# Kernel optimization log

Hardware: AMD Instinct MI355X
Metric: run time of the kernel (lower is better)

Reference implementation:

```python
import jax, jax.numpy as jnp
import numpy as np

N_HEADS = 2
HEAD_DIM = 32
SCALE = HEAD_DIM ** -0.5


def group_linear(x, w):
    # x: (S, B, din), w: (n_blocks, din_b, dout_b) block-diagonal linear
    S, B, _ = x.shape
    nb, din_b, dout_b = w.shape
    xb = x.reshape(S, B, nb, din_b)
    yb = jnp.einsum('sbnd,nde->sbne', xb, w)
    return yb.reshape(S, B, nb * dout_b)


def setup_inputs() -> dict:
    key = jax.random.key(0)
    ks = jax.random.split(key, 5)
    S, B, dim, nb = 2048, 16, 1024, 8
    block_din = dim // nb          # 128
    emb_b = HEAD_DIM * N_HEADS     # 64 per block
    x = jax.random.normal(ks[0], (S, B, dim), dtype=jnp.float32)
    wq = 0.01 * jax.random.normal(ks[1], (nb, block_din, emb_b), dtype=jnp.float32)
    wk = 0.01 * jax.random.normal(ks[2], (nb, block_din, emb_b), dtype=jnp.float32)
    wv = 0.01 * jax.random.normal(ks[3], (nb, block_din, emb_b), dtype=jnp.float32)
    wf = 0.01 * jax.random.normal(ks[4], (nb, emb_b, block_din), dtype=jnp.float32)
    return {'x': x, 'wq': wq, 'wk': wk, 'wv': wv, 'wf': wf}


def reference(x, wq, wk, wv, wf):
    S, B, dim = x.shape
    nb = wq.shape[0]
    # block-diagonal QKV projections -> (S, B, nb, n_heads, head_dim)
    q = group_linear(x, wq).reshape(S, B, nb, N_HEADS, HEAD_DIM)
    k = group_linear(x, wk).reshape(S, B, nb, N_HEADS, HEAD_DIM)
    v = group_linear(x, wv).reshape(S, B, nb, N_HEADS, HEAD_DIM)
    # attention over the n_blocks axis; heads leading: (S, B, h, nb, hd)
    q = jnp.swapaxes(q, 2, 3) * SCALE
    k = jnp.swapaxes(k, 2, 3)
    v = jnp.swapaxes(v, 2, 3)
    score = jnp.einsum('sbhnd,sbhmd->sbhnm', q, k)  # (S,B,h,nb,nb)
    score = jax.nn.softmax(score, axis=-1)
    out = jnp.einsum('sbhnm,sbhmd->sbhnd', score, v)
    out = jnp.swapaxes(out, 2, 3).reshape(S, B, nb * N_HEADS * HEAD_DIM)
    out = group_linear(out, wf)
    return out.reshape(S, B, dim)
```

## Files before the change

kernel.cpp:

```cpp
#include <hip/hip_runtime.h>
#include <math.h>

using short8  = __attribute__((ext_vector_type(8))) short;
using ushort8 = __attribute__((ext_vector_type(8))) unsigned short;
using f32x4   = __attribute__((ext_vector_type(4))) float;

constexpr int DIM = 1024, NB = 8, NH = 2, HD = 32;
constexpr float SCALE = 0.17677669529663687f;
constexpr int SXW = 1032;
constexpr int SQW = 1544;

__device__ __forceinline__ unsigned short f2bf(float f) {
  unsigned u = __float_as_uint(f);
  u += 0x7fff + ((u >> 16) & 1);
  return (unsigned short)(u >> 16);
}
__device__ __forceinline__ float bf2f(unsigned short h) {
  return __uint_as_float((unsigned)h << 16);
}

__global__ __launch_bounds__(256) void prep_weights(
    const float* __restrict__ wq, const float* __restrict__ wk,
    const float* __restrict__ wv, const float* __restrict__ wf,
    unsigned short* __restrict__ ws)
{
  int gid = blockIdx.x * 256 + threadIdx.x;
  if (gid < 196608) {
    int t = gid >> 11, r = gid & 2047;
    int s = r >> 9, l = (r >> 3) & 63, z = r & 7;
    int met = t >> 3, n = t & 7, m = met >> 2, et = met & 3;
    int fr = l & 15, fg = l >> 4;
    int e = et * 16 + fr, k = s * 32 + fg * 8 + z;
    const float* w = (m == 0) ? wq : (m == 1) ? wk : wv;
    float v = w[n * 8192 + k * 64 + e];
    if (m == 0) v *= SCALE;
    ws[gid] = f2bf(v);
  } else {
    int g2 = gid - 196608;
    int t = g2 >> 10, r = g2 & 1023;
    int s = r >> 9, l = (r >> 3) & 63, z = r & 7;
    int n = t >> 3, et = t & 7;
    int fr = l & 15, fg = l >> 4;
    int eo = et * 16 + fr, k = s * 32 + fg * 8 + z;
    ws[gid] = f2bf(wf[n * 8192 + k * 128 + eo]);
  }
}

__global__ __launch_bounds__(512, 4) void gc_fused(
    const float* __restrict__ x,
    const unsigned short* __restrict__ wsw,
    const unsigned short* __restrict__ wsf,
    float* __restrict__ out)
{
  __shared__ __align__(16) unsigned short smem[16 * SQW];
  __shared__ float spT[16][NH][NB][NB + 1];

  const int tid  = threadIdx.x;
  const int lane = tid & 63;
  const int w    = tid >> 6;
  const int fr   = lane & 15;
  const int fg   = lane >> 4;
  const long tok0 = (long)blockIdx.x * 16;

  {
    const float* xb = x + tok0 * DIM;
    float4 xa[4], xc[4];
    #pragma unroll
    for (int jj = 0; jj < 4; ++jj) {
      int chunk = tid + 512 * jj;
      const float* src = xb + (long)(chunk >> 7) * DIM + (chunk & 127) * 8;
      xa[jj] = *reinterpret_cast<const float4*>(src);
      xc[jj] = *reinterpret_cast<const float4*>(src + 4);
    }
    #pragma unroll
    for (int jj = 0; jj < 4; ++jj) {
      int chunk = tid + 512 * jj;
      ushort8 v;
      v[0] = f2bf(xa[jj].x); v[1] = f2bf(xa[jj].y);
      v[2] = f2bf(xa[jj].z); v[3] = f2bf(xa[jj].w);
      v[4] = f2bf(xc[jj].x); v[5] = f2bf(xc[jj].y);
      v[6] = f2bf(xc[jj].z); v[7] = f2bf(xc[jj].w);
      *reinterpret_cast<ushort8*>(&smem[(chunk >> 7) * SXW + (chunk & 127) * 8]) = v;
    }
  }
  __syncthreads();

  ushort4 qreg[12];
  {
    short8 wfr[2][4];
    const unsigned short* wp0 = wsw + (w * 12) * 2048 + lane * 8;
    #pragma unroll
    for (int s = 0; s < 4; ++s)
      wfr[0][s] = *reinterpret_cast<const short8*>(wp0 + s * 512);
    #pragma unroll
    for (int j = 0; j < 12; ++j) {
      const int cc = w * 12 + j;
      const int n  = cc & 7;
      if (j < 11) {
        const unsigned short* wpn = wsw + (cc + 1) * 2048 + lane * 8;
        #pragma unroll
        for (int s = 0; s < 4; ++s)
          wfr[(j + 1) & 1][s] = *reinterpret_cast<const short8*>(wpn + s * 512);
      }
      short8 bfr[4];
      #pragma unroll
      for (int s = 0; s < 4; ++s)
        bfr[s] = *reinterpret_cast<const short8*>(&smem[fr * SXW + n * 128 + s * 32 + fg * 8]);
      f32x4 acc = {0.f, 0.f, 0.f, 0.f};
      #pragma unroll
      for (int s = 0; s < 4; ++s)
        acc = __builtin_amdgcn_mfma_f32_16x16x32_bf16(wfr[j & 1][s], bfr[s], acc, 0, 0, 0);
      ushort4 d4;
      d4.x = f2bf(acc[0]); d4.y = f2bf(acc[1]);
      d4.z = f2bf(acc[2]); d4.w = f2bf(acc[3]);
      qreg[j] = d4;
    }
  }
  __syncthreads();
  {
    #pragma unroll
    for (int j = 0; j < 12; ++j) {
      const int cc = w * 12 + j;
      const int met = cc >> 3, n = cc & 7;
      const int m = met >> 2, e0 = (met & 3) * 16;
      *reinterpret_cast<ushort4*>(&smem[fr * SQW + m * 512 + n * 64 + e0 + fg * 4]) = qreg[j];
    }
  }
  __syncthreads();

  {
    const int la = lane & 15, ga = lane >> 4;
    const int rowoff = (la & 7) * 64 + (la >> 3) * 32;
    const bool useful = ((ga >> 1) == (la >> 3));
    #pragma unroll
    for (int tt = 0; tt < 2; ++tt) {
      const int t = w * 2 + tt;
      const unsigned short* tb = &smem[t * SQW];
      short8 kfr = *reinterpret_cast<const short8*>(tb + 512 + rowoff + ga * 8);
      short8 qfr = *reinterpret_cast<const short8*>(tb + rowoff + ga * 8);
      f32x4 zero = {0.f, 0.f, 0.f, 0.f};
      f32x4 s = __builtin_amdgcn_mfma_f32_16x16x32_bf16(kfr, qfr, zero, 0, 0, 0);
      float m4 = fmaxf(fmaxf(s[0], s[1]), fmaxf(s[2], s[3]));
      float mx = fmaxf(m4, __shfl_xor(m4, 16));
      float e0 = __expf(s[0] - mx), e1 = __expf(s[1] - mx);
      float e2 = __expf(s[2] - mx), e3 = __expf(s[3] - mx);
      float sm  = e0 + e1 + e2 + e3;
      float smt = sm + __shfl_xor(sm, 16);
      if (useful) {
        const float inv = 1.f / smt;
        const int h = la >> 3, nq = la & 7, m0 = (ga & 1) * 4;
        spT[t][h][m0 + 0][nq] = e0 * inv;
        spT[t][h][m0 + 1][nq] = e1 * inv;
        spT[t][h][m0 + 2][nq] = e2 * inv;
        spT[t][h][m0 + 3][nq] = e3 * inv;
      }
    }
  }
  __syncthreads();

  if (tid < 256) {
    const int t = tid >> 4;
    const int h = (tid >> 3) & 1;
    const int g = tid & 7;
    float acc[NB][4] = {};
    #pragma unroll
    for (int m = 0; m < NB; ++m) {
      ushort4 vv = *reinterpret_cast<const ushort4*>(
          &smem[t * SQW + 1024 + m * 64 + h * 32 + g * 4]);
      float v0 = bf2f(vv.x), v1 = bf2f(vv.y), v2 = bf2f(vv.z), v3 = bf2f(vv.w);
      const float* pr = spT[t][h][m];
      #pragma unroll
      for (int nn = 0; nn < NB; ++nn) {
        float p = pr[nn];
        acc[nn][0] = fmaf(p, v0, acc[nn][0]);
        acc[nn][1] = fmaf(p, v1, acc[nn][1]);
        acc[nn][2] = fmaf(p, v2, acc[nn][2]);
        acc[nn][3] = fmaf(p, v3, acc[nn][3]);
      }
    }
    #pragma unroll
    for (int nn = 0; nn < NB; ++nn) {
      ushort4 b;
      b.x = f2bf(acc[nn][0]); b.y = f2bf(acc[nn][1]);
      b.z = f2bf(acc[nn][2]); b.w = f2bf(acc[nn][3]);
      *reinterpret_cast<ushort4*>(&smem[t * SQW + nn * 64 + h * 32 + g * 4]) = b;
    }
  }
  __syncthreads();

  {
    const int n = w;
    short8 bfr[2];
    #pragma unroll
    for (int s = 0; s < 2; ++s)
      bfr[s] = *reinterpret_cast<const short8*>(&smem[fr * SQW + n * 64 + s * 32 + fg * 8]);
    #pragma unroll
    for (int et = 0; et < 8; ++et) {
      const unsigned short* wp = wsf + (n * 8 + et) * 1024 + lane * 8;
      f32x4 acc = {0.f, 0.f, 0.f, 0.f};
      #pragma unroll
      for (int s = 0; s < 2; ++s) {
        short8 af = *reinterpret_cast<const short8*>(wp + s * 512);
        acc = __builtin_amdgcn_mfma_f32_16x16x32_bf16(af, bfr[s], acc, 0, 0, 0);
      }
      float4 o; o.x = acc[0]; o.y = acc[1]; o.z = acc[2]; o.w = acc[3];
      *reinterpret_cast<float4*>(out + (tok0 + fr) * DIM + n * 128 + et * 16 + fg * 4) = o;
    }
  }
}

extern "C" void kernel_launch(void* const* d_in, const int* in_sizes, int n_in,
                              void* d_out, int out_size, void* d_ws, size_t ws_size,
                              hipStream_t stream) {
  const float* x  = (const float*)d_in[0];
  const float* wq = (const float*)d_in[1];
  const float* wk = (const float*)d_in[2];
  const float* wv = (const float*)d_in[3];
  const float* wf = (const float*)d_in[4];
  float* out = (float*)d_out;
  unsigned short* ws = (unsigned short*)d_ws;

  prep_weights<<<dim3(1024), dim3(256), 0, stream>>>(wq, wk, wv, wf, ws);

  const int tokens = in_sizes[0] / DIM;
  gc_fused<<<dim3(tokens / 16), dim3(512), 0, stream>>>(x, ws, ws + 196608, out);
}
```

Before: 88.21 us.

## Compute attention P·V with MFMA using register-permuted probabilities and transposed V

Stores V transposed in shared memory, packs softmax probabilities to bf16 and redistributes them across lanes with ds_bpermute, then computes the probability-times-V product with MFMA instructions inside the softmax loop. This removes the spT shared buffer, one barrier, and the scalar FMA stage that ran on only half the threads. Occupancy hint is raised from 4 to 6 blocks per CU. Risks include bank conflicts from the scalar transposed V stores and register pressure from the tighter launch bound.

```diff
diff --git a/kernel.cpp b/kernel.cpp
--- a/kernel.cpp
+++ b/kernel.cpp
@@ -17,6 +17,9 @@
 }
 __device__ __forceinline__ float bf2f(unsigned short h) {
   return __uint_as_float((unsigned)h << 16);
+}
+__device__ __forceinline__ unsigned pack2bf(float lo, float hi) {
+  return (unsigned)f2bf(lo) | ((unsigned)f2bf(hi) << 16);
 }
 
 __global__ __launch_bounds__(256) void prep_weights(
@@ -46,14 +49,13 @@
   }
 }
 
-__global__ __launch_bounds__(512, 4) void gc_fused(
+__global__ __launch_bounds__(512, 6) void gc_fused(
     const float* __restrict__ x,
     const unsigned short* __restrict__ wsw,
     const unsigned short* __restrict__ wsf,
     float* __restrict__ out)
 {
   __shared__ __align__(16) unsigned short smem[16 * SQW];
-  __shared__ float spT[16][NH][NB][NB + 1];
 
   const int tid  = threadIdx.x;
   const int lane = tid & 63;
@@ -117,13 +119,23 @@
     }
   }
   __syncthreads();
+
   {
     #pragma unroll
     for (int j = 0; j < 12; ++j) {
       const int cc = w * 12 + j;
       const int met = cc >> 3, n = cc & 7;
       const int m = met >> 2, e0 = (met & 3) * 16;
-      *reinterpret_cast<ushort4*>(&smem[fr * SQW + m * 512 + n * 64 + e0 + fg * 4]) = qreg[j];
+      if (m < 2) {
+        *reinterpret_cast<ushort4*>(&smem[fr * SQW + m * 512 + n * 64 + e0 + fg * 4]) = qreg[j];
+      } else {
+        const unsigned short vals[4] = {qreg[j].x, qreg[j].y, qreg[j].z, qreg[j].w};
+        #pragma unroll
+        for (int r = 0; r < 4; ++r) {
+          int e = e0 + fg * 4 + r, dd = e & 31, h = e >> 5;
+          smem[fr * SQW + 1024 + dd * 16 + h * 8 + n] = vals[r];
+        }
+      }
     }
   }
   __syncthreads();
@@ -132,6 +144,8 @@
     const int la = lane & 15, ga = lane >> 4;
     const int rowoff = (la & 7) * 64 + (la >> 3) * 32;
     const bool useful = ((ga >> 1) == (la >> 3));
+    const bool kvalid = (ga < 2);
+    const int srcA = (ga * 32 + la) & 63;
     #pragma unroll
     for (int tt = 0; tt < 2; ++tt) {
       const int t = w * 2 + tt;
@@ -146,44 +160,26 @@
       float e2 = __expf(s[2] - mx), e3 = __expf(s[3] - mx);
       float sm  = e0 + e1 + e2 + e3;
       float smt = sm + __shfl_xor(sm, 16);
-      if (useful) {
-        const float inv = 1.f / smt;
-        const int h = la >> 3, nq = la & 7, m0 = (ga & 1) * 4;
-        spT[t][h][m0 + 0][nq] = e0 * inv;
-        spT[t][h][m0 + 1][nq] = e1 * inv;
-        spT[t][h][m0 + 2][nq] = e2 * inv;
-        spT[t][h][m0 + 3][nq] = e3 * inv;
-      }
-    }
-  }
-  __syncthreads();
-
-  if (tid < 256) {
-    const int t = tid >> 4;
-    const int h = (tid >> 3) & 1;
-    const int g = tid & 7;
-    float acc[NB][4] = {};
-    #pragma unroll
-    for (int m = 0; m < NB; ++m) {
-      ushort4 vv = *reinterpret_cast<const ushort4*>(
-          &smem[t * SQW + 1024 + m * 64 + h * 32 + g * 4]);
-      float v0 = bf2f(vv.x), v1 = bf2f(vv.y), v2 = bf2f(vv.z), v3 = bf2f(vv.w);
-      const float* pr = spT[t][h][m];
-      #pragma unroll
-      for (int nn = 0; nn < NB; ++nn) {
-        float p = pr[nn];
-        acc[nn][0] = fmaf(p, v0, acc[nn][0]);
-        acc[nn][1] = fmaf(p, v1, acc[nn][1]);
-        acc[nn][2] = fmaf(p, v2, acc[nn][2]);
-        acc[nn][3] = fmaf(p, v3, acc[nn][3]);
-      }
-    }
-    #pragma unroll
-    for (int nn = 0; nn < NB; ++nn) {
-      ushort4 b;
-      b.x = f2bf(acc[nn][0]); b.y = f2bf(acc[nn][1]);
-      b.z = f2bf(acc[nn][2]); b.w = f2bf(acc[nn][3]);
-      *reinterpret_cast<ushort4*>(&smem[t * SQW + nn * 64 + h * 32 + g * 4]) = b;
+      float inv = useful ? (1.f / smt) : 0.f;
+      unsigned pk01 = pack2bf(e0 * inv, e1 * inv);
+      unsigned pk23 = pack2bf(e2 * inv, e3 * inv);
+      unsigned b0 = (unsigned)__builtin_amdgcn_ds_bpermute(srcA * 4, (int)pk01);
+      unsigned b1 = (unsigned)__builtin_amdgcn_ds_bpermute(srcA * 4, (int)pk23);
+      unsigned b2 = (unsigned)__builtin_amdgcn_ds_bpermute(((srcA + 16) & 63) * 4, (int)pk01);
+      unsigned b3 = (unsigned)__builtin_amdgcn_ds_bpermute(((srcA + 16) & 63) * 4, (int)pk23);
+      union { unsigned u[4]; short8 s8; } pb;
+      pb.u[0] = kvalid ? b0 : 0u;  pb.u[1] = kvalid ? b1 : 0u;
+      pb.u[2] = kvalid ? b2 : 0u;  pb.u[3] = kvalid ? b3 : 0u;
+      #pragma unroll
+      for (int dh = 0; dh < 2; ++dh) {
+        short8 va = *reinterpret_cast<const short8*>(
+            tb + 1024 + (dh * 16 + la) * 16 + (ga & 1) * 8);
+        f32x4 o = __builtin_amdgcn_mfma_f32_16x16x32_bf16(va, pb.s8, zero, 0, 0, 0);
+        ushort4 ou;
+        ou.x = f2bf(o[0]); ou.y = f2bf(o[1]); ou.z = f2bf(o[2]); ou.w = f2bf(o[3]);
+        *reinterpret_cast<ushort4*>(
+            &smem[t * SQW + (la & 7) * 64 + (la >> 3) * 32 + dh * 16 + ga * 4]) = ou;
+      }
     }
   }
   __syncthreads();
```

New measurement: 86.89 us, median of 2. About the same (-1.5%).
